# Kernel tuning notes

Measured on AMD Instinct MI355X. Metric: run time of the kernel, lower is better.

The kernel has to match this reference:

```python
import jax, jax.numpy as jnp
import numpy as np

B, T, N = 64, 256, 8192
D_EMB, D_ATT = 32, 128


def setup_inputs() -> dict:
    keys = iter(jax.random.split(jax.random.key(0), 64))
    nk = lambda: next(keys)
    inp = {}
    inp["x_ped"] = jax.random.normal(nk(), (B, T, 4), jnp.float32)
    inp["x_ego"] = jax.random.normal(nk(), (B, T, 4), jnp.float32)
    inp["h_ped"] = jax.random.normal(nk(), (B, D_EMB), jnp.float32)
    dims = {"neighbor": 4, "light": 6, "sign": 5, "crosswalk": 7, "station": 7}
    for name, d in dims.items():
        inp["x_" + name] = jax.random.normal(nk(), (N, T, d), jnp.float32)
        # class labels; -1 marks invalid/padded object at that timestep
        inp["cls_" + name] = jax.random.randint(nk(), (N, T), -1, 3, dtype=jnp.int32)
        inp["seg_" + name] = jnp.sort(jax.random.randint(nk(), (N,), 0, B, dtype=jnp.int32))

    def lin(din, dout):
        k1, k2 = jax.random.split(nk())
        return (jax.random.normal(k1, (din, dout), jnp.float32) / float(np.sqrt(din)),
                jax.random.normal(k2, (dout,), jnp.float32) * 0.01)

    inp["Wp"], inp["bp"] = lin(4, D_EMB)      # target_box_embedding
    inp["Wn"], inp["bn"] = lin(4, D_EMB)      # x_neighbor embedding
    inp["Wl"], inp["bl"] = lin(6, D_EMB)      # x_light
    inp["Wsi"], inp["bsi"] = lin(5, D_EMB)    # x_sign
    inp["Wc"], inp["bc"] = lin(7, D_EMB)      # x_crosswalk
    inp["Wst"], inp["bst"] = lin(7, D_EMB)    # x_station
    inp["We"], inp["be"] = lin(4, D_EMB)      # x_ego
    inp["Wax"], _ = lin(D_EMB, D_ATT)         # additive attention: value proj
    inp["Wah"], inp["ba"] = lin(D_EMB, D_ATT)  # additive attention: query proj
    inp["va"] = jax.random.normal(nk(), (D_ATT,), jnp.float32) / float(np.sqrt(D_ATT))
    inp["W1"], inp["b1"] = lin(7 * D_EMB, D_EMB)  # classifier (6 traffic types + ped)
    inp["W2"], inp["b2"] = lin(D_EMB, D_EMB)
    inp["W3"], inp["b3"] = lin(D_EMB, 1)
    inp["t"] = 8
    return inp


def _masked_segment_softmax(score, mask, seg, num_segments):
    # equals torch.exp(score)/segment_sum(exp) over valid objects, stably
    s = jnp.where(mask, score, -1e30)
    smax = jax.ops.segment_max(s, seg, num_segments=num_segments)
    smax = jnp.where(smax > -1e29, smax, 0.0)  # empty segments -> 0
    e = jnp.where(mask, jnp.exp(score - smax[seg]), 0.0)
    denom = jax.ops.segment_sum(e, seg, num_segments=num_segments)
    return e / jnp.maximum(denom[seg], 1e-30)


def _attend_type(x, cls, seg, W, b, h_ped, Wax, Wah, ba, va, t):
    emb_t = jax.nn.relu(x[:, t] @ W + b)                    # [N, 32]
    mask = cls[:, t] != -1                                   # [N]
    # additive attention score: v^T tanh(Wx*x + Wh*h + b)
    score = jnp.tanh(emb_t @ Wax + h_ped[seg] @ Wah + ba) @ va  # [N]
    probs = _masked_segment_softmax(score, mask, seg, B)     # [N], 0 where masked
    # identity-matmul scatter-add in the original == segment_sum
    feat = jax.ops.segment_sum(emb_t * probs[:, None], seg, num_segments=B)  # [B, 32]
    return feat, probs


def reference(x_ped, x_ego, h_ped,
              x_neighbor, cls_neighbor, seg_neighbor,
              x_light, cls_light, seg_light,
              x_sign, cls_sign, seg_sign,
              x_crosswalk, cls_crosswalk, seg_crosswalk,
              x_station, cls_station, seg_station,
              Wp, bp, Wn, bn, Wl, bl, Wsi, bsi, Wc, bc, Wst, bst, We, be,
              Wax, Wah, ba, va, W1, b1, W2, b2, W3, b3, t):
    ped_t = jax.nn.relu(x_ped[:, t] @ Wp + bp)               # [B, 32]
    ego_t = jax.nn.relu(x_ego[:, t] @ We + be)               # ego is a plain tensor (cls_ego is Tensor)
    f_n, p_n = _attend_type(x_neighbor, cls_neighbor, seg_neighbor, Wn, bn, h_ped, Wax, Wah, ba, va, t)
    f_l, p_l = _attend_type(x_light, cls_light, seg_light, Wl, bl, h_ped, Wax, Wah, ba, va, t)
    f_si, p_si = _attend_type(x_sign, cls_sign, seg_sign, Wsi, bsi, h_ped, Wax, Wah, ba, va, t)
    f_c, p_c = _attend_type(x_crosswalk, cls_crosswalk, seg_crosswalk, Wc, bc, h_ped, Wax, Wah, ba, va, t)
    f_st, p_st = _attend_type(x_station, cls_station, seg_station, Wst, bst, h_ped, Wax, Wah, ba, va, t)
    feats = jnp.concatenate([ped_t, f_n, f_l, f_si, f_c, f_st, ego_t], axis=-1)  # [B, 224]
    # classifier (dropout is identity in eval)
    h1 = jax.nn.relu(feats @ W1 + b1)
    h2 = jax.nn.relu(h1 @ W2 + b2)
    int_det_score = h2 @ W3 + b3                             # [B, 1]
    return int_det_score, feats, p_n, p_l, p_si, p_c, p_st
```

## Files before the change

kernel.cpp:

```cpp
#include <hip/hip_runtime.h>

#define TSTEPS 256
#define NOBJ   8192
#define BATCH  64
#define DEMB   32
#define DATT   128

#define HW_OFF     0
#define EX_OFF     32768
#define SEGOFF_OFF 196608
#define EMB_OFF    199168
#define WS_NEED    (EMB_OFF + 5 * NOBJ * DEMB * 4)

struct SP {
    const float* x[5]; const int* cls[5]; const int* seg[5];
    const float* W[5]; const float* bias[5];
    const float* x_ped; const float* x_ego; const float* h_ped;
    const float* Wp; const float* bp; const float* We; const float* be;
    const float* Wax; const float* Wah; const float* ba; const float* va;
    const float* W1; const float* b1; const float* W2; const float* b2;
    const float* W3; const float* b3;
    const int* t_ptr;
    float* out;
    float* hW;
    float* ex;
    int* seg_off;
    float* emb;
    int d[5];
    int use_emb;
};

__device__ __forceinline__ int load_t(const void* p) {
    unsigned w0 = *(const unsigned*)p;
    if (w0 < (unsigned)TSTEPS) return (int)w0;
    float f = __uint_as_float(w0);
    if (f >= 0.f && f < 256.f) return (int)f;
    return 8;
}

__device__ __forceinline__ float fast_tanh(float x) {
    float e = __expf(2.0f * x);
    return 1.0f - 2.0f / (e + 1.0f);
}

__global__ __launch_bounds__(128) void k_prep(SP p) {
    if (blockIdx.x >= BATCH) {
        const int g    = (blockIdx.x - BATCH) * 128 + threadIdx.x;
        const int type = g >> 13;
        const int i    = g & (NOBJ - 1);
        const int* __restrict__ seg = p.seg[type];
        const int sv = seg[i];
        const int pv = (i == 0) ? -1 : seg[i - 1];
        for (int v = pv + 1; v <= sv; ++v) p.seg_off[type * 65 + v] = i;
        if (i == NOBJ - 1)
            for (int v = sv + 1; v <= BATCH; ++v) p.seg_off[type * 65 + v] = NOBJ;
        return;
    }
    const int b = blockIdx.x;
    const int j = threadIdx.x;
    const int t = load_t(p.t_ptr);
    float a = p.ba[j];
    const float* h = p.h_ped + b * DEMB;
    #pragma unroll
    for (int k = 0; k < DEMB; ++k) a += h[k] * p.Wah[k * DATT + j];
    p.hW[b * DATT + j] = a;

    if (j < DEMB) {
        const float* xp = p.x_ped + (size_t)(b * TSTEPS + t) * 4;
        float e = p.bp[j];
        #pragma unroll
        for (int k = 0; k < 4; ++k) e += xp[k] * p.Wp[k * DEMB + j];
        p.out[64 + b * 224 + j] = fmaxf(e, 0.f);
        const float* xe = p.x_ego + (size_t)(b * TSTEPS + t) * 4;
        float g = p.be[j];
        #pragma unroll
        for (int k = 0; k < 4; ++k) g += xe[k] * p.We[k * DEMB + j];
        p.out[64 + b * 224 + 192 + j] = fmaxf(g, 0.f);
    }
}

template<int D>
__device__ __forceinline__ void score_body(const SP& p, const int type, const int t,
                                           float* WaxT, float* W_s, float* b_s) {
    const int tid = threadIdx.x;
    const float* __restrict__ x   = p.x[type];
    const int*   __restrict__ cls = p.cls[type];
    const int*   __restrict__ seg = p.seg[type];

    const int q = tid & 15;
    const int o = tid >> 4;
    const int i0 = blockIdx.x * 32 + o;
    const int i1 = i0 + 16;

    const int c0 = cls[i0 * TSTEPS + t];
    const int c1 = cls[i1 * TSTEPS + t];
    const int b0 = seg[i0];
    const int b1 = seg[i1];
    float xv0[D], xv1[D];
    {
        const float* xr0 = x + (size_t)(i0 * TSTEPS + t) * D;
        const float* xr1 = x + (size_t)(i1 * TSTEPS + t) * D;
        #pragma unroll
        for (int k = 0; k < D; ++k) { xv0[k] = xr0[k]; xv1[k] = xr1[k]; }
    }
    float hv0[8], hv1[8], vv[8];
    {
        const float* hp0 = p.hW + b0 * DATT + q * 8;
        const float* hp1 = p.hW + b1 * DATT + q * 8;
        const float* vp  = p.va + q * 8;
        *(float4*)(hv0)   = *(const float4*)(hp0);
        *(float4*)(hv0+4) = *(const float4*)(hp0+4);
        *(float4*)(hv1)   = *(const float4*)(hp1);
        *(float4*)(hv1+4) = *(const float4*)(hp1+4);
        *(float4*)(vv)    = *(const float4*)(vp);
        *(float4*)(vv+4)  = *(const float4*)(vp+4);
    }

    for (int i = tid; i < DATT * DEMB; i += 256) {
        const int j = i >> 5, k = i & 31;
        WaxT[i] = p.Wax[k * DATT + j];
    }
    for (int i = tid; i < D * DEMB; i += 256) W_s[i] = p.W[type][i];
    if (tid < DEMB) b_s[tid] = p.bias[type][tid];
    __syncthreads();

    float acc0[8], acc1[8];
    #pragma unroll
    for (int jo = 0; jo < 8; ++jo) { acc0[jo] = 0.f; acc1[jo] = 0.f; }

    const float4* b4 = (const float4*)b_s;
    #pragma unroll
    for (int cc = 0; cc < 8; ++cc) {
        const int c = (cc + q) & 7;
        float4 a0 = b4[c], a1 = b4[c];
        #pragma unroll
        for (int k = 0; k < D; ++k) {
            const float4 w = *(const float4*)&W_s[k * DEMB + 4 * c];
            a0.x += xv0[k]*w.x; a0.y += xv0[k]*w.y; a0.z += xv0[k]*w.z; a0.w += xv0[k]*w.w;
            a1.x += xv1[k]*w.x; a1.y += xv1[k]*w.y; a1.z += xv1[k]*w.z; a1.w += xv1[k]*w.w;
        }
        a0.x = fmaxf(a0.x, 0.f); a0.y = fmaxf(a0.y, 0.f);
        a0.z = fmaxf(a0.z, 0.f); a0.w = fmaxf(a0.w, 0.f);
        a1.x = fmaxf(a1.x, 0.f); a1.y = fmaxf(a1.y, 0.f);
        a1.z = fmaxf(a1.z, 0.f); a1.w = fmaxf(a1.w, 0.f);

        if (p.use_emb && cc == 0 && q < 8) {
            p.emb[((size_t)type * NOBJ + i0) * DEMB + 4 * q + 0] = a0.x;
            *(float4*)&p.emb[((size_t)type * NOBJ + i0) * DEMB + 4 * q] = a0;
            *(float4*)&p.emb[((size_t)type * NOBJ + i1) * DEMB + 4 * q] = a1;
        }
        #pragma unroll
        for (int jo = 0; jo < 8; ++jo) {
            const float4 w = *(const float4*)&WaxT[(q * 8 + jo) * DEMB + 4 * c];
            acc0[jo] += a0.x*w.x + a0.y*w.y + a0.z*w.z + a0.w*w.w;
            acc1[jo] += a1.x*w.x + a1.y*w.y + a1.z*w.z + a1.w*w.w;
        }
    }

    float sc0 = 0.f, sc1 = 0.f;
    #pragma unroll
    for (int jo = 0; jo < 8; ++jo) {
        sc0 += fast_tanh(hv0[jo] + acc0[jo]) * vv[jo];
        sc1 += fast_tanh(hv1[jo] + acc1[jo]) * vv[jo];
    }
    sc0 += __shfl_xor(sc0, 1); sc1 += __shfl_xor(sc1, 1);
    sc0 += __shfl_xor(sc0, 2); sc1 += __shfl_xor(sc1, 2);
    sc0 += __shfl_xor(sc0, 4); sc1 += __shfl_xor(sc1, 4);
    sc0 += __shfl_xor(sc0, 8); sc1 += __shfl_xor(sc1, 8);

    if (q == 0) {
        p.ex[type * NOBJ + i0] = (c0 != -1) ? __expf(sc0) : 0.f;
        p.ex[type * NOBJ + i1] = (c1 != -1) ? __expf(sc1) : 0.f;
    }
}

__global__ __launch_bounds__(256) void k_score(SP p) {
    __shared__ __align__(16) float WaxT[DATT * DEMB];
    __shared__ __align__(16) float W_s[7 * DEMB];
    __shared__ __align__(16) float b_s[DEMB];
    const int t = load_t(p.t_ptr);
    switch (blockIdx.y) {
        case 0: score_body<4>(p, 0, t, WaxT, W_s, b_s); break;
        case 1: score_body<6>(p, 1, t, WaxT, W_s, b_s); break;
        case 2: score_body<5>(p, 2, t, WaxT, W_s, b_s); break;
        case 3: score_body<7>(p, 3, t, WaxT, W_s, b_s); break;
        default: score_body<7>(p, 4, t, WaxT, W_s, b_s); break;
    }
}

__global__ __launch_bounds__(256) void k_finish(SP p) {
    const int type = blockIdx.y;
    const int bseg = blockIdx.x;
    const int tid  = threadIdx.x;
    const int j    = tid & 31;
    const int sl   = tid >> 5;
    const int wv   = tid >> 6;
    const float* __restrict__ ex = p.ex + type * NOBJ;
    const int lo = p.seg_off[type * 65 + bseg];
    const int hi = p.seg_off[type * 65 + bseg + 1];

    __shared__ float red4[4];
    __shared__ float ared[4][DEMB];

    float s = 0.f;
    for (int i = lo + tid; i < hi; i += 256) s += ex[i];
    #pragma unroll
    for (int off = 32; off; off >>= 1) s += __shfl_xor(s, off);
    if ((tid & 63) == 0) red4[wv] = s;
    __syncthreads();
    const float inv = 1.0f / fmaxf(red4[0] + red4[1] + red4[2] + red4[3], 1e-30f);

    float acc = 0.f;
    float* pout = p.out + 64 + BATCH * 224 + type * NOBJ;
    if (p.use_emb) {
        const float* __restrict__ eb = p.emb + (size_t)type * NOBJ * DEMB;
        for (int i = lo + sl; i < hi; i += 8) {
            const float pr = ex[i] * inv;
            if (j == 0) pout[i] = pr;
            acc += pr * eb[(size_t)i * DEMB + j];
        }
    } else {
        const int t = load_t(p.t_ptr);
        const int d = p.d[type];
        float wj[7];
        for (int k = 0; k < d; ++k) wj[k] = p.W[type][k * DEMB + j];
        const float bj = p.bias[type][j];
        for (int i = lo + sl; i < hi; i += 8) {
            const float e = ex[i];
            const float pr = e * inv;
            if (j == 0) pout[i] = pr;
            if (e > 0.f) {
                const float* xr = p.x[type] + (size_t)(i * TSTEPS + t) * d;
                float a = bj;
                for (int k = 0; k < d; ++k) a += xr[k] * wj[k];
                acc += pr * fmaxf(a, 0.f);
            }
        }
    }
    acc += __shfl_xor(acc, 32);
    if ((tid & 63) < 32) ared[wv][j] = acc;
    __syncthreads();
    if (tid < DEMB) {
        const float f = ared[0][tid] + ared[1][tid] + ared[2][tid] + ared[3][tid];
        p.out[64 + bseg * 224 + 32 * (1 + type) + tid] = f;
    }
}

__global__ __launch_bounds__(64) void k_head(SP p) {
    const int b   = blockIdx.x;
    const int tid = threadIdx.x;
    const int j    = tid & 31;
    const int half = tid >> 5;
    __shared__ float h1s[DEMB];
    __shared__ float h2s[DEMB];
    const float* feats = p.out + 64 + b * 224;

    float a = 0.f;
    const int k0 = half * 112;
    #pragma unroll 4
    for (int k = k0; k < k0 + 112; ++k)
        a += feats[k] * p.W1[k * DEMB + j];
    a += __shfl_xor(a, 32);
    if (half == 0) h1s[j] = fmaxf(a + p.b1[j], 0.f);
    __syncthreads();

    float a2 = 0.f;
    const int k2 = half * 16;
    #pragma unroll
    for (int k = k2; k < k2 + 16; ++k)
        a2 += h1s[k] * p.W2[k * DEMB + j];
    a2 += __shfl_xor(a2, 32);
    if (half == 0) h2s[j] = fmaxf(a2 + p.b2[j], 0.f);
    __syncthreads();

    if (half == 0) {
        float v = h2s[j] * p.W3[j];
        v += __shfl_xor(v, 16); v += __shfl_xor(v, 8);
        v += __shfl_xor(v, 4);  v += __shfl_xor(v, 2); v += __shfl_xor(v, 1);
        if (j == 0) p.out[b] = v + p.b3[0];
    }
}

extern "C" void kernel_launch(void* const* d_in, const int* in_sizes, int n_in,
                              void* d_out, int out_size, void* d_ws, size_t ws_size,
                              hipStream_t stream) {
    (void)in_sizes; (void)n_in; (void)out_size;

    SP p;
    const int xi[5] = {3, 6, 9, 12, 15};
    const int wi[5] = {20, 22, 24, 26, 28};
    const int di[5] = {4, 6, 5, 7, 7};
    for (int tp = 0; tp < 5; ++tp) {
        p.x[tp]    = (const float*)d_in[xi[tp]];
        p.cls[tp]  = (const int*)d_in[xi[tp] + 1];
        p.seg[tp]  = (const int*)d_in[xi[tp] + 2];
        p.W[tp]    = (const float*)d_in[wi[tp]];
        p.bias[tp] = (const float*)d_in[wi[tp] + 1];
        p.d[tp]    = di[tp];
    }
    p.x_ped = (const float*)d_in[0];
    p.x_ego = (const float*)d_in[1];
    p.h_ped = (const float*)d_in[2];
    p.Wp = (const float*)d_in[18]; p.bp = (const float*)d_in[19];
    p.We = (const float*)d_in[30]; p.be = (const float*)d_in[31];
    p.Wax = (const float*)d_in[32]; p.Wah = (const float*)d_in[33];
    p.ba  = (const float*)d_in[34]; p.va  = (const float*)d_in[35];
    p.W1 = (const float*)d_in[36]; p.b1 = (const float*)d_in[37];
    p.W2 = (const float*)d_in[38]; p.b2 = (const float*)d_in[39];
    p.W3 = (const float*)d_in[40]; p.b3 = (const float*)d_in[41];
    p.t_ptr = (const int*)d_in[42];
    p.out = (float*)d_out;
    char* ws = (char*)d_ws;
    p.hW      = (float*)(ws + HW_OFF);
    p.ex      = (float*)(ws + EX_OFF);
    p.seg_off = (int*)(ws + SEGOFF_OFF);
    p.emb     = (float*)(ws + EMB_OFF);
    p.use_emb = (ws_size >= (size_t)WS_NEED) ? 1 : 0;

    hipLaunchKernelGGL(k_prep,   dim3(BATCH + 5 * NOBJ / 128), dim3(128), 0, stream, p);
    hipLaunchKernelGGL(k_score,  dim3(NOBJ / 32, 5),           dim3(256), 0, stream, p);
    hipLaunchKernelGGL(k_finish, dim3(BATCH, 5),               dim3(256), 0, stream, p);
    hipLaunchKernelGGL(k_head,   dim3(BATCH),                  dim3(64),  0, stream, p);
}
```

Before: 44.78 us.

## Stage object embeddings in shared memory and score 64 objects per block

The score kernel now computes each object's ReLU embedding once per (object, column) into a padded shared-memory tile, instead of every thread recomputing the embedding redundantly. Each block now handles 64 objects with 4 objects per thread, which halves the number of blocks and amortises the per-block transpose of Wax into shared memory over more objects. The prep kernel is widened to 256 threads. In exchange there is extra shared memory, a larger accumulator register footprint, and fewer blocks in flight.

Measured after the change: 45.21 us. Within noise of the previous version (+1.0%).

```diff
diff --git a/kernel.cpp b/kernel.cpp
--- a/kernel.cpp
+++ b/kernel.cpp
@@ -43,9 +43,9 @@
     return 1.0f - 2.0f / (e + 1.0f);
 }
 
-__global__ __launch_bounds__(128) void k_prep(SP p) {
+__global__ __launch_bounds__(256) void k_prep(SP p) {
     if (blockIdx.x >= BATCH) {
-        const int g    = (blockIdx.x - BATCH) * 128 + threadIdx.x;
+        const int g    = (blockIdx.x - BATCH) * 256 + threadIdx.x;
         const int type = g >> 13;
         const int i    = g & (NOBJ - 1);
         const int* __restrict__ seg = p.seg[type];
@@ -59,12 +59,13 @@
     const int b = blockIdx.x;
     const int j = threadIdx.x;
     const int t = load_t(p.t_ptr);
-    float a = p.ba[j];
-    const float* h = p.h_ped + b * DEMB;
-    #pragma unroll
-    for (int k = 0; k < DEMB; ++k) a += h[k] * p.Wah[k * DATT + j];
-    p.hW[b * DATT + j] = a;
-
+    if (j < DATT) {
+        float a = p.ba[j];
+        const float* h = p.h_ped + b * DEMB;
+        #pragma unroll
+        for (int k = 0; k < DEMB; ++k) a += h[k] * p.Wah[k * DATT + j];
+        p.hW[b * DATT + j] = a;
+    }
     if (j < DEMB) {
         const float* xp = p.x_ped + (size_t)(b * TSTEPS + t) * 4;
         float e = p.bp[j];
@@ -79,112 +80,109 @@
     }
 }
 
+#define EPAD 36
 template<int D>
 __device__ __forceinline__ void score_body(const SP& p, const int type, const int t,
-                                           float* WaxT, float* W_s, float* b_s) {
+                                           float* WaxT, float* embS) {
     const int tid = threadIdx.x;
     const float* __restrict__ x   = p.x[type];
     const int*   __restrict__ cls = p.cls[type];
     const int*   __restrict__ seg = p.seg[type];
-
+    const int blkbase = blockIdx.x * 64;
+
+    const int s = tid >> 4;
     const int q = tid & 15;
-    const int o = tid >> 4;
-    const int i0 = blockIdx.x * 32 + o;
-    const int i1 = i0 + 16;
-
-    const int c0 = cls[i0 * TSTEPS + t];
-    const int c1 = cls[i1 * TSTEPS + t];
-    const int b0 = seg[i0];
-    const int b1 = seg[i1];
-    float xv0[D], xv1[D];
-    {
-        const float* xr0 = x + (size_t)(i0 * TSTEPS + t) * D;
-        const float* xr1 = x + (size_t)(i1 * TSTEPS + t) * D;
-        #pragma unroll
-        for (int k = 0; k < D; ++k) { xv0[k] = xr0[k]; xv1[k] = xr1[k]; }
-    }
-    float hv0[8], hv1[8], vv[8];
-    {
-        const float* hp0 = p.hW + b0 * DATT + q * 8;
-        const float* hp1 = p.hW + b1 * DATT + q * 8;
-        const float* vp  = p.va + q * 8;
-        *(float4*)(hv0)   = *(const float4*)(hp0);
-        *(float4*)(hv0+4) = *(const float4*)(hp0+4);
-        *(float4*)(hv1)   = *(const float4*)(hp1);
-        *(float4*)(hv1+4) = *(const float4*)(hp1+4);
-        *(float4*)(vv)    = *(const float4*)(vp);
-        *(float4*)(vv+4)  = *(const float4*)(vp+4);
-    }
-
-    for (int i = tid; i < DATT * DEMB; i += 256) {
-        const int j = i >> 5, k = i & 31;
-        WaxT[i] = p.Wax[k * DATT + j];
-    }
-    for (int i = tid; i < D * DEMB; i += 256) W_s[i] = p.W[type][i];
-    if (tid < DEMB) b_s[tid] = p.bias[type][tid];
-    __syncthreads();
-
-    float acc0[8], acc1[8];
-    #pragma unroll
-    for (int jo = 0; jo < 8; ++jo) { acc0[jo] = 0.f; acc1[jo] = 0.f; }
-
-    const float4* b4 = (const float4*)b_s;
+
+    int bseg[4], cv[4];
+    #pragma unroll
+    for (int po = 0; po < 4; ++po) {
+        const int i = blkbase + s + 16 * po;
+        bseg[po] = seg[i];
+        cv[po]   = cls[i * TSTEPS + t];
+    }
+
+    for (int idx = tid; idx < DATT * DEMB; idx += 256) {
+        const int j = idx >> 5, k = idx & 31;
+        WaxT[idx] = p.Wax[k * DATT + j];
+    }
+    const float* __restrict__ Wt = p.W[type];
+    const float* __restrict__ bt = p.bias[type];
+    float* __restrict__ embg = p.emb + ((size_t)type * NOBJ + blkbase) * DEMB;
+    for (int idx = tid; idx < 64 * DEMB; idx += 256) {
+        const int o = idx >> 5, col = idx & 31;
+        const float* xr = x + (size_t)((blkbase + o) * TSTEPS + t) * D;
+        float a = bt[col];
+        #pragma unroll
+        for (int k = 0; k < D; ++k) a += xr[k] * Wt[k * DEMB + col];
+        a = fmaxf(a, 0.f);
+        embS[o * EPAD + col] = a;
+        if (p.use_emb) embg[idx] = a;
+    }
+    __syncthreads();
+
+    float acc[4][8];
+    #pragma unroll
+    for (int po = 0; po < 4; ++po)
+        #pragma unroll
+        for (int jo = 0; jo < 8; ++jo) acc[po][jo] = 0.f;
+
     #pragma unroll
     for (int cc = 0; cc < 8; ++cc) {
-        const int c = (cc + q) & 7;
-        float4 a0 = b4[c], a1 = b4[c];
-        #pragma unroll
-        for (int k = 0; k < D; ++k) {
-            const float4 w = *(const float4*)&W_s[k * DEMB + 4 * c];
-            a0.x += xv0[k]*w.x; a0.y += xv0[k]*w.y; a0.z += xv0[k]*w.z; a0.w += xv0[k]*w.w;
-            a1.x += xv1[k]*w.x; a1.y += xv1[k]*w.y; a1.z += xv1[k]*w.z; a1.w += xv1[k]*w.w;
+        const int ch = (cc + q) & 7;
+        const float4 e0 = *(const float4*)&embS[(s     ) * EPAD + 4 * ch];
+        const float4 e1 = *(const float4*)&embS[(s + 16) * EPAD + 4 * ch];
+        const float4 e2 = *(const float4*)&embS[(s + 32) * EPAD + 4 * ch];
+        const float4 e3 = *(const float4*)&embS[(s + 48) * EPAD + 4 * ch];
+        #pragma unroll
+        for (int jo = 0; jo < 8; ++jo) {
+            const float4 w = *(const float4*)&WaxT[(q * 8 + jo) * DEMB + 4 * ch];
+            acc[0][jo] += e0.x*w.x + e0.y*w.y + e0.z*w.z + e0.w*w.w;
+            acc[1][jo] += e1.x*w.x + e1.y*w.y + e1.z*w.z + e1.w*w.w;
+            acc[2][jo] += e2.x*w.x + e2.y*w.y + e2.z*w.z + e2.w*w.w;
+            acc[3][jo] += e3.x*w.x + e3.y*w.y + e3.z*w.z + e3.w*w.w;
         }
-        a0.x = fmaxf(a0.x, 0.f); a0.y = fmaxf(a0.y, 0.f);
-        a0.z = fmaxf(a0.z, 0.f); a0.w = fmaxf(a0.w, 0.f);
-        a1.x = fmaxf(a1.x, 0.f); a1.y = fmaxf(a1.y, 0.f);
-        a1.z = fmaxf(a1.z, 0.f); a1.w = fmaxf(a1.w, 0.f);
-
-        if (p.use_emb && cc == 0 && q < 8) {
-            p.emb[((size_t)type * NOBJ + i0) * DEMB + 4 * q + 0] = a0.x;
-            *(float4*)&p.emb[((size_t)type * NOBJ + i0) * DEMB + 4 * q] = a0;
-            *(float4*)&p.emb[((size_t)type * NOBJ + i1) * DEMB + 4 * q] = a1;
-        }
-        #pragma unroll
-        for (int jo = 0; jo < 8; ++jo) {
-            const float4 w = *(const float4*)&WaxT[(q * 8 + jo) * DEMB + 4 * c];
-            acc0[jo] += a0.x*w.x + a0.y*w.y + a0.z*w.z + a0.w*w.w;
-            acc1[jo] += a1.x*w.x + a1.y*w.y + a1.z*w.z + a1.w*w.w;
-        }
-    }
-
-    float sc0 = 0.f, sc1 = 0.f;
-    #pragma unroll
-    for (int jo = 0; jo < 8; ++jo) {
-        sc0 += fast_tanh(hv0[jo] + acc0[jo]) * vv[jo];
-        sc1 += fast_tanh(hv1[jo] + acc1[jo]) * vv[jo];
-    }
-    sc0 += __shfl_xor(sc0, 1); sc1 += __shfl_xor(sc1, 1);
-    sc0 += __shfl_xor(sc0, 2); sc1 += __shfl_xor(sc1, 2);
-    sc0 += __shfl_xor(sc0, 4); sc1 += __shfl_xor(sc1, 4);
-    sc0 += __shfl_xor(sc0, 8); sc1 += __shfl_xor(sc1, 8);
-
+    }
+
+    float vv[8];
+    *(float4*)(vv)     = *(const float4*)(p.va + q * 8);
+    *(float4*)(vv + 4) = *(const float4*)(p.va + q * 8 + 4);
+    float sc[4];
+    #pragma unroll
+    for (int po = 0; po < 4; ++po) {
+        float hv[8];
+        const float* hp = p.hW + bseg[po] * DATT + q * 8;
+        *(float4*)(hv)     = *(const float4*)(hp);
+        *(float4*)(hv + 4) = *(const float4*)(hp + 4);
+        float v = 0.f;
+        #pragma unroll
+        for (int jo = 0; jo < 8; ++jo)
+            v += fast_tanh(hv[jo] + acc[po][jo]) * vv[jo];
+        sc[po] = v;
+    }
+    #pragma unroll
+    for (int po = 0; po < 4; ++po) {
+        sc[po] += __shfl_xor(sc[po], 1);
+        sc[po] += __shfl_xor(sc[po], 2);
+        sc[po] += __shfl_xor(sc[po], 4);
+        sc[po] += __shfl_xor(sc[po], 8);
+    }
     if (q == 0) {
-        p.ex[type * NOBJ + i0] = (c0 != -1) ? __expf(sc0) : 0.f;
-        p.ex[type * NOBJ + i1] = (c1 != -1) ? __expf(sc1) : 0.f;
+        #pragma unroll
+        for (int po = 0; po < 4; ++po)
+            p.ex[type * NOBJ + blkbase + s + 16 * po] = (cv[po] != -1) ? __expf(sc[po]) : 0.f;
     }
 }
 
 __global__ __launch_bounds__(256) void k_score(SP p) {
     __shared__ __align__(16) float WaxT[DATT * DEMB];
-    __shared__ __align__(16) float W_s[7 * DEMB];
-    __shared__ __align__(16) float b_s[DEMB];
+    __shared__ __align__(16) float embS[64 * EPAD];
     const int t = load_t(p.t_ptr);
     switch (blockIdx.y) {
-        case 0: score_body<4>(p, 0, t, WaxT, W_s, b_s); break;
-        case 1: score_body<6>(p, 1, t, WaxT, W_s, b_s); break;
-        case 2: score_body<5>(p, 2, t, WaxT, W_s, b_s); break;
-        case 3: score_body<7>(p, 3, t, WaxT, W_s, b_s); break;
-        default: score_body<7>(p, 4, t, WaxT, W_s, b_s); break;
+        case 0: score_body<4>(p, 0, t, WaxT, embS); break;
+        case 1: score_body<6>(p, 1, t, WaxT, embS); break;
+        case 2: score_body<5>(p, 2, t, WaxT, embS); break;
+        case 3: score_body<7>(p, 3, t, WaxT, embS); break;
+        default: score_body<7>(p, 4, t, WaxT, embS); break;
     }
 }
 
@@ -317,8 +315,8 @@
     p.emb     = (float*)(ws + EMB_OFF);
     p.use_emb = (ws_size >= (size_t)WS_NEED) ? 1 : 0;
 
-    hipLaunchKernelGGL(k_prep,   dim3(BATCH + 5 * NOBJ / 128), dim3(128), 0, stream, p);
-    hipLaunchKernelGGL(k_score,  dim3(NOBJ / 32, 5),           dim3(256), 0, stream, p);
-    hipLaunchKernelGGL(k_finish, dim3(BATCH, 5),               dim3(256), 0, stream, p);
-    hipLaunchKernelGGL(k_head,   dim3(BATCH),                  dim3(64),  0, stream, p);
-}
+    hipLaunchKernelGGL(k_prep,   dim3(BATCH + 160),  dim3(256), 0, stream, p);
+    hipLaunchKernelGGL(k_score,  dim3(NOBJ / 64, 5), dim3(256), 0, stream, p);
+    hipLaunchKernelGGL(k_finish, dim3(BATCH, 5),     dim3(256), 0, stream, p);
+    hipLaunchKernelGGL(k_head,   dim3(BATCH),        dim3(64),  0, stream, p);
+}
```

## Fuse segment softmax-pooling and classifier head into one per-batch kernel

Applied to the files above, without the earlier changes.

Replaces the k_finish grid (64x5 blocks) and the separate k_head launch with a single k_fin kernel that uses one block per batch element. Each block loops over the five object types, keeps the 224-wide feature row in shared memory, and then runs the three-layer classifier directly from that row. This removes one kernel launch and a global-memory round-trip of the features, and it also drops a redundant scalar store in k_score and widens k_prep blocks to 256 threads. The cost is fewer blocks working on the pooling stage (64 instead of 320), which serialises the five types within each block.

Result: slower. 65.66 us (+46.6%).

```diff
diff --git a/kernel.cpp b/kernel.cpp
--- a/kernel.cpp
+++ b/kernel.cpp
@@ -43,9 +43,9 @@
     return 1.0f - 2.0f / (e + 1.0f);
 }
 
-__global__ __launch_bounds__(128) void k_prep(SP p) {
+__global__ __launch_bounds__(256) void k_prep(SP p) {
     if (blockIdx.x >= BATCH) {
-        const int g    = (blockIdx.x - BATCH) * 128 + threadIdx.x;
+        const int g    = (blockIdx.x - BATCH) * 256 + threadIdx.x;
         const int type = g >> 13;
         const int i    = g & (NOBJ - 1);
         const int* __restrict__ seg = p.seg[type];
@@ -59,12 +59,13 @@
     const int b = blockIdx.x;
     const int j = threadIdx.x;
     const int t = load_t(p.t_ptr);
-    float a = p.ba[j];
-    const float* h = p.h_ped + b * DEMB;
-    #pragma unroll
-    for (int k = 0; k < DEMB; ++k) a += h[k] * p.Wah[k * DATT + j];
-    p.hW[b * DATT + j] = a;
-
+    if (j < DATT) {
+        float a = p.ba[j];
+        const float* h = p.h_ped + b * DEMB;
+        #pragma unroll
+        for (int k = 0; k < DEMB; ++k) a += h[k] * p.Wah[k * DATT + j];
+        p.hW[b * DATT + j] = a;
+    }
     if (j < DEMB) {
         const float* xp = p.x_ped + (size_t)(b * TSTEPS + t) * 4;
         float e = p.bp[j];
@@ -145,7 +146,6 @@
         a1.z = fmaxf(a1.z, 0.f); a1.w = fmaxf(a1.w, 0.f);
 
         if (p.use_emb && cc == 0 && q < 8) {
-            p.emb[((size_t)type * NOBJ + i0) * DEMB + 4 * q + 0] = a0.x;
             *(float4*)&p.emb[((size_t)type * NOBJ + i0) * DEMB + 4 * q] = a0;
             *(float4*)&p.emb[((size_t)type * NOBJ + i1) * DEMB + 4 * q] = a1;
         }
@@ -188,96 +188,110 @@
     }
 }
 
-__global__ __launch_bounds__(256) void k_finish(SP p) {
-    const int type = blockIdx.y;
-    const int bseg = blockIdx.x;
-    const int tid  = threadIdx.x;
-    const int j    = tid & 31;
-    const int sl   = tid >> 5;
-    const int wv   = tid >> 6;
-    const float* __restrict__ ex = p.ex + type * NOBJ;
-    const int lo = p.seg_off[type * 65 + bseg];
-    const int hi = p.seg_off[type * 65 + bseg + 1];
-
+__global__ __launch_bounds__(256) void k_fin(SP p) {
+    const int b   = blockIdx.x;
+    const int tid = threadIdx.x;
+    const int j   = tid & 31;
+    const int sl  = tid >> 5;
+    const int wv  = tid >> 6;
+    const int t   = load_t(p.t_ptr);
+
+    __shared__ float feats_s[224];
     __shared__ float red4[4];
     __shared__ float ared[4][DEMB];
-
-    float s = 0.f;
-    for (int i = lo + tid; i < hi; i += 256) s += ex[i];
-    #pragma unroll
-    for (int off = 32; off; off >>= 1) s += __shfl_xor(s, off);
-    if ((tid & 63) == 0) red4[wv] = s;
-    __syncthreads();
-    const float inv = 1.0f / fmaxf(red4[0] + red4[1] + red4[2] + red4[3], 1e-30f);
-
-    float acc = 0.f;
-    float* pout = p.out + 64 + BATCH * 224 + type * NOBJ;
-    if (p.use_emb) {
-        const float* __restrict__ eb = p.emb + (size_t)type * NOBJ * DEMB;
-        for (int i = lo + sl; i < hi; i += 8) {
-            const float pr = ex[i] * inv;
-            if (j == 0) pout[i] = pr;
-            acc += pr * eb[(size_t)i * DEMB + j];
-        }
-    } else {
-        const int t = load_t(p.t_ptr);
-        const int d = p.d[type];
-        float wj[7];
-        for (int k = 0; k < d; ++k) wj[k] = p.W[type][k * DEMB + j];
-        const float bj = p.bias[type][j];
-        for (int i = lo + sl; i < hi; i += 8) {
-            const float e = ex[i];
-            const float pr = e * inv;
-            if (j == 0) pout[i] = pr;
-            if (e > 0.f) {
-                const float* xr = p.x[type] + (size_t)(i * TSTEPS + t) * d;
-                float a = bj;
-                for (int k = 0; k < d; ++k) a += xr[k] * wj[k];
-                acc += pr * fmaxf(a, 0.f);
+    __shared__ float h1s[DEMB], h2s[DEMB];
+
+    if (tid < 64) {
+        const bool ego = tid >= 32;
+        const float* xr = (ego ? p.x_ego : p.x_ped) + (size_t)(b * TSTEPS + t) * 4;
+        const float* W  = ego ? p.We : p.Wp;
+        const float* bb = ego ? p.be : p.bp;
+        float a = bb[j];
+        #pragma unroll
+        for (int k = 0; k < 4; ++k) a += xr[k] * W[k * DEMB + j];
+        a = fmaxf(a, 0.f);
+        const int col = ego ? 192 + j : j;
+        feats_s[col] = a;
+        p.out[64 + b * 224 + col] = a;
+    }
+
+    for (int type = 0; type < 5; ++type) {
+        const float* __restrict__ ex = p.ex + type * NOBJ;
+        const int lo = p.seg_off[type * 65 + b];
+        const int hi = p.seg_off[type * 65 + b + 1];
+
+        float s = 0.f;
+        for (int i = lo + tid; i < hi; i += 256) s += ex[i];
+        #pragma unroll
+        for (int off = 32; off; off >>= 1) s += __shfl_xor(s, off);
+        if ((tid & 63) == 0) red4[wv] = s;
+        __syncthreads();
+        const float inv = 1.0f / fmaxf(red4[0] + red4[1] + red4[2] + red4[3], 1e-30f);
+
+        float acc = 0.f;
+        float* pout = p.out + 64 + BATCH * 224 + type * NOBJ;
+        if (p.use_emb) {
+            const float* __restrict__ eb = p.emb + (size_t)type * NOBJ * DEMB;
+            for (int i = lo + sl; i < hi; i += 8) {
+                const float pr = ex[i] * inv;
+                if (j == 0) pout[i] = pr;
+                acc += pr * eb[(size_t)i * DEMB + j];
             }
-        }
-    }
-    acc += __shfl_xor(acc, 32);
-    if ((tid & 63) < 32) ared[wv][j] = acc;
+        } else {
+            const int d = p.d[type];
+            float wj[7];
+            for (int k = 0; k < d; ++k) wj[k] = p.W[type][k * DEMB + j];
+            const float bj = p.bias[type][j];
+            for (int i = lo + sl; i < hi; i += 8) {
+                const float e = ex[i];
+                const float pr = e * inv;
+                if (j == 0) pout[i] = pr;
+                if (e > 0.f) {
+                    const float* xr = p.x[type] + (size_t)(i * TSTEPS + t) * d;
+                    float a = bj;
+                    for (int k = 0; k < d; ++k) a += xr[k] * wj[k];
+                    acc += pr * fmaxf(a, 0.f);
+                }
+            }
+        }
+        acc += __shfl_xor(acc, 32);
+        __syncthreads();
+        if ((tid & 63) < 32) ared[wv][j] = acc;
+        __syncthreads();
+        if (tid < DEMB) {
+            const float f = ared[0][tid] + ared[1][tid] + ared[2][tid] + ared[3][tid];
+            feats_s[32 + type * 32 + tid] = f;
+            p.out[64 + b * 224 + 32 * (1 + type) + tid] = f;
+        }
+    }
+    __syncthreads();
+
+    float a1 = 0.f;
+    {
+        const int k0 = sl * 28;
+        #pragma unroll 4
+        for (int k = k0; k < k0 + 28; ++k)
+            a1 += feats_s[k] * p.W1[k * DEMB + j];
+    }
+    a1 += __shfl_xor(a1, 32);
+    __syncthreads();
+    if ((tid & 63) < 32) ared[wv][j] = a1;
+    __syncthreads();
+    if (tid < DEMB)
+        h1s[tid] = fmaxf(ared[0][tid] + ared[1][tid] + ared[2][tid] + ared[3][tid] + p.b1[tid], 0.f);
     __syncthreads();
     if (tid < DEMB) {
-        const float f = ared[0][tid] + ared[1][tid] + ared[2][tid] + ared[3][tid];
-        p.out[64 + bseg * 224 + 32 * (1 + type) + tid] = f;
-    }
-}
-
-__global__ __launch_bounds__(64) void k_head(SP p) {
-    const int b   = blockIdx.x;
-    const int tid = threadIdx.x;
-    const int j    = tid & 31;
-    const int half = tid >> 5;
-    __shared__ float h1s[DEMB];
-    __shared__ float h2s[DEMB];
-    const float* feats = p.out + 64 + b * 224;
-
-    float a = 0.f;
-    const int k0 = half * 112;
-    #pragma unroll 4
-    for (int k = k0; k < k0 + 112; ++k)
-        a += feats[k] * p.W1[k * DEMB + j];
-    a += __shfl_xor(a, 32);
-    if (half == 0) h1s[j] = fmaxf(a + p.b1[j], 0.f);
-    __syncthreads();
-
-    float a2 = 0.f;
-    const int k2 = half * 16;
-    #pragma unroll
-    for (int k = k2; k < k2 + 16; ++k)
-        a2 += h1s[k] * p.W2[k * DEMB + j];
-    a2 += __shfl_xor(a2, 32);
-    if (half == 0) h2s[j] = fmaxf(a2 + p.b2[j], 0.f);
-    __syncthreads();
-
-    if (half == 0) {
-        float v = h2s[j] * p.W3[j];
+        float a2 = p.b2[tid];
+        #pragma unroll
+        for (int k = 0; k < DEMB; ++k) a2 += h1s[k] * p.W2[k * DEMB + tid];
+        h2s[tid] = fmaxf(a2, 0.f);
+    }
+    __syncthreads();
+    if (tid < DEMB) {
+        float v = h2s[tid] * p.W3[tid];
         v += __shfl_xor(v, 16); v += __shfl_xor(v, 8);
         v += __shfl_xor(v, 4);  v += __shfl_xor(v, 2); v += __shfl_xor(v, 1);
-        if (j == 0) p.out[b] = v + p.b3[0];
+        if (tid == 0) p.out[b] = v + p.b3[0];
     }
 }
 
@@ -317,8 +331,7 @@
     p.emb     = (float*)(ws + EMB_OFF);
     p.use_emb = (ws_size >= (size_t)WS_NEED) ? 1 : 0;
 
-    hipLaunchKernelGGL(k_prep,   dim3(BATCH + 5 * NOBJ / 128), dim3(128), 0, stream, p);
-    hipLaunchKernelGGL(k_score,  dim3(NOBJ / 32, 5),           dim3(256), 0, stream, p);
-    hipLaunchKernelGGL(k_finish, dim3(BATCH, 5),               dim3(256), 0, stream, p);
-    hipLaunchKernelGGL(k_head,   dim3(BATCH),                  dim3(64),  0, stream, p);
-}
+    hipLaunchKernelGGL(k_prep,  dim3(BATCH + 160),  dim3(256), 0, stream, p);
+    hipLaunchKernelGGL(k_score, dim3(NOBJ / 32, 5), dim3(256), 0, stream, p);
+    hipLaunchKernelGGL(k_fin,   dim3(BATCH),        dim3(256), 0, stream, p);
+}
```
